# Performance work log

Measured on AMD Instinct MI355X. Metric: run time of the kernel, lower is better.

## Reference

```python
import jax, jax.numpy as jnp
import numpy as np

N, E, B, STEPS, THETAS, F, R = 20000, 40000, 32, 32, 64, 3, 1.0


def setup_inputs() -> dict:
    key = jax.random.key(0)
    k1, k2, k3, k4 = jax.random.split(key, 4)
    x = jax.random.normal(k1, (N, F), dtype=jnp.float32)
    v = jax.random.normal(k2, (F, THETAS), dtype=jnp.float32)
    v = v / jnp.linalg.norm(v, axis=0, keepdims=True)  # sphere constraint on directions
    lin = jnp.linspace(-R, R, STEPS, dtype=jnp.float32)
    edge_index = jax.random.randint(k3, (2, E), 0, N, dtype=jnp.int64)
    batch = jnp.sort(jax.random.randint(k4, (N,), 0, B, dtype=jnp.int64))
    return {"x": x, "v": v, "lin": lin, "edge_index": edge_index, "batch": batch}


def _ecc(h, idx, lin, num_segments):
    # h: [M, T] heights; idx: [M] graph ids; lin: [S] thresholds
    # sigmoid(200*(lin - h)) -> [M, S, T], then segment-sum over M -> [B, S, T]
    e = jax.nn.sigmoid(200.0 * (lin[None, :, None] - h[:, None, :]))
    return jax.ops.segment_sum(e, idx, num_segments=num_segments)


def reference(x, v, lin, edge_index, batch):
    nh = x @ v                                            # [N, T] node heights
    eh = jnp.maximum(nh[edge_index[0]], nh[edge_index[1]])  # [E, T] edge heights (max of endpoints)
    edge_batch = batch[edge_index[0]]                     # [E]
    ect_nodes = _ecc(nh, batch, lin, B)                   # [B, S, T]
    ect_edges = _ecc(eh, edge_batch, lin, B)              # [B, S, T]
    return ect_nodes - ect_edges / 2
```

## Files before the change

kernel.cpp:

```cpp
#include <hip/hip_runtime.h>

#define N_NODES 20000
#define N_EDGES 40000
#define NB 32
#define NS 32
#define NT 64
#define NSC 160
#define NPREP 180
#define CAPB 1536
#define KBM 32
#define NBLKM (NB * KBM)
#define CH 8
#define SEG (NS * NT)
#define STEP200 12.9032258065f
#define WB 0.496f


__device__ __forceinline__ float bcast(float x, int j) {
    return __uint_as_float(__builtin_amdgcn_readlane(__float_as_uint(x), j));
}

__device__ __forceinline__ void accum_item(float h, float w, int lane,
                                           float* __restrict__ acc,
                                           float* __restrict__ fdiff) {
    const float t200h = 200.0f * h;
    const float u = (h + 1.0f) * 15.5f;
    const int kb = (int)ceilf(u - WB);
    const int ke = (int)floorf(u + WB) + 1;
#pragma unroll
    for (int j = 0; j < 2; j++) {
        const int s = kb + j;
        if (s < ke && s >= 0 && s < NS) {
            const float z = fmaf((float)s, STEP200, -200.0f) - t200h;
            const float sig = __builtin_amdgcn_rcpf(1.0f + __expf(-z));
            atomicAdd(&acc[s * NT + lane], w * sig);
        }
    }
    const int kec = min(max(ke, 0), NS);
    atomicAdd(&fdiff[kec * NT + lane], w);
}

__global__ __launch_bounds__(256) void prep_kernel(
        const float* __restrict__ x, const int* __restrict__ ei,
        const int* __restrict__ batch, int* __restrict__ ecnt,
        int* __restrict__ node_base, float4* __restrict__ sedge) {
    const int t = threadIdx.x;
    const int bid = blockIdx.x;

    if (bid < NSC) {
        __shared__ int h[NB];
        __shared__ int basep[NB];
        if (t < NB) h[t] = 0;
        __syncthreads();
        const int e = bid * 256 + t;
        int b = -1, s = 0, d = 0;
        if (e < N_EDGES) {
            s = ei[e];
            d = ei[N_EDGES + e];
            b = batch[s];
            atomicAdd(&h[b], 1);
        }
        __syncthreads();
        if (t < NB && h[t] > 0) {
            basep[t] = atomicAdd(&ecnt[t], h[t]);
            h[t] = 0;
        }
        __syncthreads();
        if (b >= 0) {
            const int p = atomicAdd(&h[b], 1);
            const int g = basep[b] + p;
            if (g < CAPB) {
                float4* ep = sedge + (size_t)(b * CAPB + g) * 2;
                ep[0] = make_float4(x[3 * s], x[3 * s + 1], x[3 * s + 2], x[3 * d]);
                ep[1] = make_float4(x[3 * d + 1], x[3 * d + 2], 0.0f, 0.0f);
            }
        }
    } else {
#pragma unroll
        for (int k = 0; k < 4; k++) {
            const int n = (bid - NSC) * 1024 + k * 256 + t;
            if (n < N_NODES) {
                const int bn = batch[n];
                const int bp = (n == 0) ? -1 : batch[n - 1];
                for (int q = bp + 1; q <= bn; q++) node_base[q] = n;
                if (n == N_NODES - 1)
                    for (int q = bn + 1; q <= NB; q++) node_base[q] = N_NODES;
            }
        }
    }
}

__global__ __launch_bounds__(512) void ect_main_kernel(
        const float* __restrict__ x, const float* __restrict__ v,
        const int* __restrict__ node_base, const int* __restrict__ ecnt,
        const float4* __restrict__ sedge, float* __restrict__ part) {
    __shared__ float acc[SEG];
    __shared__ float fdiff[(NS + 1) * NT];
    const int t = threadIdx.x;
#pragma unroll
    for (int j = 0; j < 4; j++) acc[t + 512 * j] = 0.0f;
    for (int idx = t; idx < (NS + 1) * NT; idx += 512) fdiff[idx] = 0.0f;
    __syncthreads();

    const int lane = t & 63;
    const int wid = __builtin_amdgcn_readfirstlane(t >> 6);
    const int b = blockIdx.x / KBM;
    const int slot = (blockIdx.x % KBM) * 8 + wid;
    const float v0 = v[lane], v1 = v[NT + lane], v2 = v[2 * NT + lane];

    const int nlo = node_base[b], nhi = node_base[b + 1];
    const int nn = nhi - nlo;
    const int ne = min(ecnt[b], CAPB);
    const int cn = (nn + CH - 1) / CH;
    const int ce = (ne + CH - 1) / CH;

    for (int c = slot; c < cn + ce; c += KBM * 8) {
        if (c < cn) {
            const int base = nlo + c * CH;
            const int cnt = min(nhi - base, CH);
            const int li = base + min(lane & (CH - 1), cnt - 1);
            const float ax = x[3 * li], ay = x[3 * li + 1], az = x[3 * li + 2];
            for (int j = 0; j < cnt; j++) {
                const float h = fmaf(bcast(ax, j), v0,
                                fmaf(bcast(ay, j), v1, bcast(az, j) * v2));
                accum_item(h, 1.0f, lane, acc, fdiff);
            }
        } else {
            const int base = (c - cn) * CH;
            const int cnt = min(ne - base, CH);
            const int li = b * CAPB + base + min(lane & (CH - 1), cnt - 1);
            const float4* ep = sedge + (size_t)li * 2;
            const float4 A = ep[0], Bv = ep[1];
            for (int j = 0; j < cnt; j++) {
                const float hs = fmaf(bcast(A.x, j), v0,
                                 fmaf(bcast(A.y, j), v1, bcast(A.z, j) * v2));
                const float hd = fmaf(bcast(A.w, j), v0,
                                 fmaf(bcast(Bv.x, j), v1, bcast(Bv.y, j) * v2));
                accum_item(fmaxf(hs, hd), -0.5f, lane, acc, fdiff);
            }
        }
    }
    __syncthreads();

    if (t < NT) {
        float run = 0.0f;
#pragma unroll
        for (int s = 0; s < NS; s++) {
            run += fdiff[s * NT + t];
            acc[s * NT + t] += run;
        }
    }
    __syncthreads();

    const float4* a4 = (const float4*)acc;
    float4* pb = (float4*)(part + (size_t)blockIdx.x * SEG);
    pb[t] = a4[t];
}

__global__ __launch_bounds__(256) void reduce_kernel(
        const float* __restrict__ part, float* __restrict__ out) {
    const int o4 = blockIdx.x * 256 + threadIdx.x;
    const int b = o4 >> 9;
    const int i4 = o4 & 511;
    const float4* p = (const float4*)(part + (size_t)b * KBM * SEG) + i4;
    float4 s = p[0];
#pragma unroll
    for (int k = 1; k < KBM; k++) {
        const float4 q = p[k * (SEG / 4)];
        s.x += q.x; s.y += q.y; s.z += q.z; s.w += q.w;
    }
    ((float4*)out)[o4] = s;
}

extern "C" void kernel_launch(void* const* d_in, const int* in_sizes, int n_in,
                              void* d_out, int out_size, void* d_ws, size_t ws_size,
                              hipStream_t stream) {
    const float* x   = (const float*)d_in[0];
    const float* v   = (const float*)d_in[1];
    const int*   ei  = (const int*)d_in[3];
    const int*   bat = (const int*)d_in[4];

    float* out = (float*)d_out;

    int* ecnt      = (int*)d_ws;
    int* node_base = ecnt + NB;
    float4* sedge  = (float4*)((int*)d_ws + 72);
    float* part    = (float*)((int*)d_ws + 72 + NB * CAPB * 8);

    hipMemsetAsync(ecnt, 0, NB * sizeof(int), stream);
    prep_kernel<<<NPREP, 256, 0, stream>>>(x, ei, bat, ecnt, node_base, sedge);
    ect_main_kernel<<<NBLKM, 512, 0, stream>>>(x, v, node_base, ecnt, sedge, part);
    reduce_kernel<<<64, 256, 0, stream>>>(part, out);
}
```

Before: 109.9 us.

## Approximate sigmoid with single nearest step and fuse reduction via global atomics

The per-item work drops from up to two sigmoid evaluations and two shared atomics to one sigmoid at the nearest threshold plus the step-function diff. The separate reduce kernel and partial buffer are removed: output is zeroed in the prep kernel and each block atomically adds its nonzero accumulator entries directly into the output. KBM drops to 8 blocks per graph and the chunk size rises to 32, so each block handles more items and there are fewer partials to combine. This drops the second sigmoid term, which changes numerics slightly, and adds global atomic contention on the output in exchange for one fewer launch.

```diff
diff --git a/kernel.cpp b/kernel.cpp
--- a/kernel.cpp
+++ b/kernel.cpp
@@ -8,12 +8,11 @@
 #define NSC 160
 #define NPREP 180
 #define CAPB 1536
-#define KBM 32
+#define KBM 8
 #define NBLKM (NB * KBM)
-#define CH 8
+#define CH 32
 #define SEG (NS * NT)
 #define STEP200 12.9032258065f
-#define WB 0.496f
 
 
 __device__ __forceinline__ float bcast(float x, int j) {
@@ -23,29 +22,27 @@
 __device__ __forceinline__ void accum_item(float h, float w, int lane,
                                            float* __restrict__ acc,
                                            float* __restrict__ fdiff) {
-    const float t200h = 200.0f * h;
-    const float u = (h + 1.0f) * 15.5f;
-    const int kb = (int)ceilf(u - WB);
-    const int ke = (int)floorf(u + WB) + 1;
-#pragma unroll
-    for (int j = 0; j < 2; j++) {
-        const int s = kb + j;
-        if (s < ke && s >= 0 && s < NS) {
-            const float z = fmaf((float)s, STEP200, -200.0f) - t200h;
-            const float sig = __builtin_amdgcn_rcpf(1.0f + __expf(-z));
-            atomicAdd(&acc[s * NT + lane], w * sig);
-        }
-    }
-    const int kec = min(max(ke, 0), NS);
+    const float u = fmaf(h, 15.5f, 15.5f);
+    const float s0f = rintf(u);
+    const int s0 = (int)s0f;
+    const float e = __expf((u - s0f) * STEP200);
+    const float sig = __builtin_amdgcn_rcpf(1.0f + e);
+    const int sc = min(max(s0, 0), NS - 1);
+    const float val = (s0 == sc) ? w * sig : 0.0f;
+    atomicAdd(&acc[sc * NT + lane], val);
+    const int kec = min(max(s0 + 1, 0), NS);
     atomicAdd(&fdiff[kec * NT + lane], w);
 }
 
 __global__ __launch_bounds__(256) void prep_kernel(
         const float* __restrict__ x, const int* __restrict__ ei,
         const int* __restrict__ batch, int* __restrict__ ecnt,
-        int* __restrict__ node_base, float4* __restrict__ sedge) {
+        int* __restrict__ node_base, float4* __restrict__ sedge,
+        float* __restrict__ out_zero) {
     const int t = threadIdx.x;
     const int bid = blockIdx.x;
+    for (int idx = bid * 256 + t; idx < NB * NS * NT; idx += NPREP * 256)
+        out_zero[idx] = 0.0f;
 
     if (bid < NSC) {
         __shared__ int h[NB];
@@ -93,7 +90,7 @@
 __global__ __launch_bounds__(512) void ect_main_kernel(
         const float* __restrict__ x, const float* __restrict__ v,
         const int* __restrict__ node_base, const int* __restrict__ ecnt,
-        const float4* __restrict__ sedge, float* __restrict__ part) {
+        const float4* __restrict__ sedge, float* __restrict__ out) {
     __shared__ float acc[SEG];
     __shared__ float fdiff[(NS + 1) * NT];
     const int t = threadIdx.x;
@@ -152,24 +149,13 @@
     }
     __syncthreads();
 
-    const float4* a4 = (const float4*)acc;
-    float4* pb = (float4*)(part + (size_t)blockIdx.x * SEG);
-    pb[t] = a4[t];
-}
-
-__global__ __launch_bounds__(256) void reduce_kernel(
-        const float* __restrict__ part, float* __restrict__ out) {
-    const int o4 = blockIdx.x * 256 + threadIdx.x;
-    const int b = o4 >> 9;
-    const int i4 = o4 & 511;
-    const float4* p = (const float4*)(part + (size_t)b * KBM * SEG) + i4;
-    float4 s = p[0];
+    float* ob = out + b * SEG;
 #pragma unroll
-    for (int k = 1; k < KBM; k++) {
-        const float4 q = p[k * (SEG / 4)];
-        s.x += q.x; s.y += q.y; s.z += q.z; s.w += q.w;
+    for (int j = 0; j < 4; j++) {
+        const int idx = t + 512 * j;
+        const float val = acc[idx];
+        if (val != 0.0f) atomicAdd(&ob[idx], val);
     }
-    ((float4*)out)[o4] = s;
 }
 
 extern "C" void kernel_launch(void* const* d_in, const int* in_sizes, int n_in,
@@ -185,10 +171,8 @@
     int* ecnt      = (int*)d_ws;
     int* node_base = ecnt + NB;
     float4* sedge  = (float4*)((int*)d_ws + 72);
-    float* part    = (float*)((int*)d_ws + 72 + NB * CAPB * 8);
 
     hipMemsetAsync(ecnt, 0, NB * sizeof(int), stream);
-    prep_kernel<<<NPREP, 256, 0, stream>>>(x, ei, bat, ecnt, node_base, sedge);
-    ect_main_kernel<<<NBLKM, 512, 0, stream>>>(x, v, node_base, ecnt, sedge, part);
-    reduce_kernel<<<64, 256, 0, stream>>>(part, out);
+    prep_kernel<<<NPREP, 256, 0, stream>>>(x, ei, bat, ecnt, node_base, sedge, out);
+    ect_main_kernel<<<NBLKM, 512, 0, stream>>>(x, v, node_base, ecnt, sedge, out);
 }
```

After: 111.1 us. Within noise of the previous version (+1.1%).
